# Kernel optimization log

Hardware: AMD Instinct MI355X
Metric: run time of the kernel (lower is better)

## Reference

```python
import jax, jax.numpy as jnp
import numpy as np

B, D, H, W = 512, 32, 128, 128


def setup_inputs() -> dict:
    key = jax.random.key(0)
    k1, k2, k3, k4 = jax.random.split(key, 4)
    inputs = jax.random.uniform(k1, (B, D), dtype=jnp.float32)
    stamp = jax.random.uniform(k2, (H, W, 1), dtype=jnp.float32)
    rows = jax.random.randint(k3, (D,), 0, H)
    cols = jax.random.randint(k4, (D,), 0, W)
    coords = jnp.stack([rows, cols], axis=-1).astype(jnp.int32)  # [D,2]
    return {"inputs": inputs, "stamp": stamp, "coords": coords}


def _static_indices(d, h, w):
    # rows/cols replication counts (static, numpy)
    rows_per = np.full(d, h // d, np.int32); rows_per[: h % d] += 1
    cols_per = np.full(d, w // d, np.int32); cols_per[: w % d] += 1
    # equidistant bar layout
    bar_w = w // (3 * d + 2)
    total_gap = w - d * bar_w
    gap = total_gap // (d + 1)
    extra = total_gap - gap * (d + 1)
    beg = extra // 2
    col_to_bar = np.full(w, -1, np.int32)
    for i in range(d):
        s = beg + i * (bar_w + gap) + gap
        col_to_bar[s : s + bar_w] = i
    return rows_per, cols_per, col_to_bar


def reference(inputs, stamp, coords):
    b, d = inputs.shape
    h, w = stamp.shape[:2]
    rows_per, cols_per, col_to_bar = _static_indices(d, h, w)

    # channel 1: deepinsight scatter (duplicates sum, matching tf.scatter_nd)
    di = jnp.zeros((b, h, w), inputs.dtype).at[:, coords[:, 0], coords[:, 1]].add(inputs)

    # channel 2: row-wise copy
    row_idx = np.repeat(np.arange(d), rows_per)  # [h]
    rowcopy = jnp.broadcast_to(inputs[:, row_idx][:, :, None], (b, h, w))

    # channel 3: normalized pairwise abs distance, expanded to h x w
    dm = jnp.abs(inputs[:, :, None] - inputs[:, None, :])  # [b,d,d]
    mn = jnp.min(dm, axis=(1, 2), keepdims=True)
    mx = jnp.max(dm, axis=(1, 2), keepdims=True)
    nd = (dm - mn) / (mx - mn)
    nd = nd[:, np.repeat(np.arange(d), rows_per), :][:, :, np.repeat(np.arange(d), cols_per)]

    # channel 4: equidistant bar graph (bars fill rows [0, bar_height))
    bar_height = jnp.clip(jnp.round(inputs * h).astype(jnp.int32), 0, h)  # [b,d]
    mask = (jnp.arange(h)[None, :, None] < bar_height[:, None, :]).astype(inputs.dtype)  # [b,h,d]
    safe = np.where(col_to_bar < 0, 0, col_to_bar)
    bars = mask[:, :, safe] * (col_to_bar >= 0).astype(inputs.dtype)[None, None, :]  # [b,h,w]

    stamp_b = jnp.broadcast_to(stamp, (b, h, w, 1))
    return jnp.concatenate(
        [stamp_b, di[..., None], rowcopy[..., None], nd[..., None], bars[..., None]], axis=-1
    )
```

## Files before the change

### kernel.cpp

```cpp
#include <hip/hip_runtime.h>


__global__ __launch_bounds__(256) void di_main(const float* __restrict__ inputs,
                                               const float* __restrict__ stamp,
                                               const int* __restrict__ coords,
                                               float* __restrict__ out) {
    const int blk = blockIdx.x;
    const int b = blk >> 4;
    const int part = blk & 15;
    const int tid = threadIdx.x;

    __shared__ float xs[32];
    __shared__ int bh[32];
    __shared__ float sinv;
    __shared__ float buf[256 * 20];

    if (tid < 64) {
        float v = inputs[b * 32 + (tid & 31)];
        if (tid < 32) {
            xs[tid] = v;
            int t = (int)rintf(v * 128.0f);
            bh[tid] = t < 0 ? 0 : (t > 128 ? 128 : t);
        }
        float mn = v, mx = v;
#pragma unroll
        for (int off = 1; off < 32; off <<= 1) {
            mn = fminf(mn, __shfl_xor(mn, off));
            mx = fmaxf(mx, __shfl_xor(mx, off));
        }
        if (tid == 0) sinv = 1.0f / (mx - mn);
    }
    __syncthreads();

    const float inv = sinv;

    const int lp = part * 1024 + tid * 4;
    const int h = lp >> 7;
    const int w0 = lp & 127;

    const float rowv = xs[h >> 2];
    const float ndv = fabsf(rowv - xs[w0 >> 2]) * inv;

    const float4 sv = *reinterpret_cast<const float4*>(stamp + h * 128 + w0);
    const float svj[4] = {sv.x, sv.y, sv.z, sv.w};

    alignas(16) float vals[20];
#pragma unroll
    for (int j = 0; j < 4; ++j) {
        const int w = w0 + j;
        float barv = 0.0f;
        const int t = w - 17;
        if (t >= 0 && t <= 93 && (t % 3) == 0) {
            const int bar = t / 3;
            barv = (h < bh[bar]) ? 1.0f : 0.0f;
        }
        vals[5 * j + 0] = svj[j];
        vals[5 * j + 1] = 0.0f;
        vals[5 * j + 2] = rowv;
        vals[5 * j + 3] = ndv;
        vals[5 * j + 4] = barv;
    }

    float4* lw = reinterpret_cast<float4*>(&buf[tid * 20]);
    const float4* src = reinterpret_cast<const float4*>(vals);
#pragma unroll
    for (int k = 0; k < 5; ++k) lw[k] = src[k];
    __syncthreads();

    if (tid < 32) {
        const int r = coords[2 * tid], c = coords[2 * tid + 1];
        if ((r >> 3) == part)
            atomicAdd(&buf[((r & 7) * 128 + c) * 5 + 1], xs[tid]);
    }
    __syncthreads();

    float4* dst = reinterpret_cast<float4*>(out + ((size_t)b * 16384 + (size_t)part * 1024) * 5);
    const float4* lr = reinterpret_cast<const float4*>(buf);
#pragma unroll
    for (int it = 0; it < 5; ++it) {
        const int f = it * 256 + tid;
        dst[f] = lr[f];
    }
}

extern "C" void kernel_launch(void* const* d_in, const int* in_sizes, int n_in,
                              void* d_out, int out_size, void* d_ws, size_t ws_size,
                              hipStream_t stream) {
    const float* inputs = (const float*)d_in[0];
    const float* stamp  = (const float*)d_in[1];
    const int*   coords = (const int*)d_in[2];
    float* out = (float*)d_out;

    di_main<<<8192, 256, 0, stream>>>(inputs, stamp, coords, out);
}
```

Baseline: 167.7 us.

## Write interleaved output directly from registers, dropping LDS staging buffer

Removes the 20 KB shared-memory staging buffer. Each thread now computes every output float4 directly by decoding pixel and channel from the flat index, then stores it straight to global memory. Each block covers a quarter-image (20 float4 per thread) instead of 1/16, which cuts the grid from 8192 to 2048 blocks. Duplicate-coordinate scatter adds are done with global atomics after a barrier. The trade is more per-element index arithmetic and branching, plus scalar stamp loads, in exchange for less LDS traffic and higher occupancy. Correctness relies on the global stores being visible to the same block's atomics after __syncthreads.

```diff
diff --git a/kernel.cpp b/kernel.cpp
--- a/kernel.cpp
+++ b/kernel.cpp
@@ -6,14 +6,13 @@
                                                const int* __restrict__ coords,
                                                float* __restrict__ out) {
     const int blk = blockIdx.x;
-    const int b = blk >> 4;
-    const int part = blk & 15;
+    const int b = blk >> 2;
+    const int qt = blk & 3;
     const int tid = threadIdx.x;
 
     __shared__ float xs[32];
     __shared__ int bh[32];
     __shared__ float sinv;
-    __shared__ float buf[256 * 20];
 
     if (tid < 64) {
         float v = inputs[b * 32 + (tid & 31)];
@@ -31,55 +30,52 @@
         if (tid == 0) sinv = 1.0f / (mx - mn);
     }
     __syncthreads();
-
     const float inv = sinv;
 
-    const int lp = part * 1024 + tid * 4;
-    const int h = lp >> 7;
-    const int w0 = lp & 127;
+    float4* outq = reinterpret_cast<float4*>(out) + (size_t)b * 20480 + (size_t)qt * 5120;
 
-    const float rowv = xs[h >> 2];
-    const float ndv = fabsf(rowv - xs[w0 >> 2]) * inv;
+#pragma unroll 2
+    for (int i = 0; i < 20; ++i) {
+        const int q = i * 256 + tid;
+        const unsigned F = (unsigned)(qt * 5120 + q) * 4u;
+        unsigned p = F / 5u;
+        int ch = (int)(F - p * 5u);
 
-    const float4 sv = *reinterpret_cast<const float4*>(stamp + h * 128 + w0);
-    const float svj[4] = {sv.x, sv.y, sv.z, sv.w};
+        float vjs[4];
+#pragma unroll
+        for (int j = 0; j < 4; ++j) {
+            const int h = (int)(p >> 7);
+            const int w = (int)(p & 127u);
+            const float rowv = xs[h >> 2];
+            const float ndv = fabsf(rowv - xs[w >> 2]) * inv;
+            const int t = w - 17;
+            const int bar = t / 3;
+            float barv = 0.0f;
+            if (t >= 0 && t - bar * 3 == 0 && bar < 32)
+                barv = (h < bh[bar]) ? 1.0f : 0.0f;
+            const float sval = stamp[p];
 
-    alignas(16) float vals[20];
-#pragma unroll
-    for (int j = 0; j < 4; ++j) {
-        const int w = w0 + j;
-        float barv = 0.0f;
-        const int t = w - 17;
-        if (t >= 0 && t <= 93 && (t % 3) == 0) {
-            const int bar = t / 3;
-            barv = (h < bh[bar]) ? 1.0f : 0.0f;
+            float val;
+            if (ch == 0)      val = sval;
+            else if (ch == 1) val = 0.0f;
+            else if (ch == 2) val = rowv;
+            else if (ch == 3) val = ndv;
+            else              val = barv;
+            vjs[j] = val;
+
+            ++ch;
+            if (ch == 5) { ch = 0; ++p; }
         }
-        vals[5 * j + 0] = svj[j];
-        vals[5 * j + 1] = 0.0f;
-        vals[5 * j + 2] = rowv;
-        vals[5 * j + 3] = ndv;
-        vals[5 * j + 4] = barv;
+        float4 r;
+        r.x = vjs[0]; r.y = vjs[1]; r.z = vjs[2]; r.w = vjs[3];
+        outq[q] = r;
     }
 
-    float4* lw = reinterpret_cast<float4*>(&buf[tid * 20]);
-    const float4* src = reinterpret_cast<const float4*>(vals);
-#pragma unroll
-    for (int k = 0; k < 5; ++k) lw[k] = src[k];
     __syncthreads();
-
     if (tid < 32) {
         const int r = coords[2 * tid], c = coords[2 * tid + 1];
-        if ((r >> 3) == part)
-            atomicAdd(&buf[((r & 7) * 128 + c) * 5 + 1], xs[tid]);
-    }
-    __syncthreads();
-
-    float4* dst = reinterpret_cast<float4*>(out + ((size_t)b * 16384 + (size_t)part * 1024) * 5);
-    const float4* lr = reinterpret_cast<const float4*>(buf);
-#pragma unroll
-    for (int it = 0; it < 5; ++it) {
-        const int f = it * 256 + tid;
-        dst[f] = lr[f];
+        if ((r >> 5) == qt)
+            atomicAdd(out + ((size_t)b * 16384 + (size_t)(r * 128 + c)) * 5 + 1, xs[tid]);
     }
 }
 
@@ -91,5 +87,5 @@
     const int*   coords = (const int*)d_in[2];
     float* out = (float*)d_out;
 
-    di_main<<<8192, 256, 0, stream>>>(inputs, stamp, coords, out);
+    di_main<<<2048, 256, 0, stream>>>(inputs, stamp, coords, out);
 }
```

New measurement: 199.4 us. +18.9%, slower.

## Process two chunks per block with double-buffered LDS and shuffle-based broadcasts

Applied to the files above, without the earlier changes.

Each block now handles two 1024-pixel chunks, using two LDS buffers so the second chunk is computed while the first is written out. Per-batch values (inputs, bar heights, min/max) are kept in registers and broadcast with wave shuffles rather than through shared memory, which removes the initial barrier. The duplicate-summing scatter now issues global atomics after the stores, with a final block barrier to order them within the block. The grid is halved, which lowers occupancy, and the global atomics rely on that block-level ordering against its own earlier stores.

```diff
diff --git a/kernel.cpp b/kernel.cpp
--- a/kernel.cpp
+++ b/kernel.cpp
@@ -6,80 +6,80 @@
                                                const int* __restrict__ coords,
                                                float* __restrict__ out) {
     const int blk = blockIdx.x;
-    const int b = blk >> 4;
-    const int part = blk & 15;
+    const int b = blk >> 3;
+    const int part = blk & 7;
     const int tid = threadIdx.x;
+    const int lane = tid & 63;
 
-    __shared__ float xs[32];
-    __shared__ int bh[32];
-    __shared__ float sinv;
-    __shared__ float buf[256 * 20];
+    __shared__ float buf[2][256 * 20];
 
-    if (tid < 64) {
-        float v = inputs[b * 32 + (tid & 31)];
-        if (tid < 32) {
-            xs[tid] = v;
-            int t = (int)rintf(v * 128.0f);
-            bh[tid] = t < 0 ? 0 : (t > 128 ? 128 : t);
+    const float v = inputs[b * 32 + (lane & 31)];
+    int bt = (int)rintf(v * 128.0f);
+    bt = bt < 0 ? 0 : (bt > 128 ? 128 : bt);
+    float mn = v, mx = v;
+#pragma unroll
+    for (int off = 1; off < 32; off <<= 1) {
+        mn = fminf(mn, __shfl_xor(mn, off));
+        mx = fmaxf(mx, __shfl_xor(mx, off));
+    }
+    const float inv = 1.0f / (mx - mn);
+
+    auto compute = [&](int c, float* vals) {
+        const int lp = part * 2048 + c * 1024 + tid * 4;
+        const int h = lp >> 7;
+        const int w0 = lp & 127;
+        const float rowv = __shfl(v, h >> 2);
+        const float ndv = fabsf(rowv - __shfl(v, w0 >> 2)) * inv;
+        const float4 sv = *reinterpret_cast<const float4*>(stamp + h * 128 + w0);
+        const float svj[4] = {sv.x, sv.y, sv.z, sv.w};
+#pragma unroll
+        for (int j = 0; j < 4; ++j) {
+            const int w = w0 + j;
+            const int t = w - 17;
+            const int bar = t / 3;
+            const bool valid = (t >= 0) && (t <= 93) && (t - bar * 3 == 0);
+            const int bhv = __shfl(bt, valid ? bar : 0);
+            const float barv = (valid && h < bhv) ? 1.0f : 0.0f;
+            vals[5 * j + 0] = svj[j];
+            vals[5 * j + 1] = 0.0f;
+            vals[5 * j + 2] = rowv;
+            vals[5 * j + 3] = ndv;
+            vals[5 * j + 4] = barv;
         }
-        float mn = v, mx = v;
+    };
+    auto stage = [&](int c, const float* vals) {
+        float4* lw = reinterpret_cast<float4*>(&buf[c][tid * 20]);
+        const float4* src = reinterpret_cast<const float4*>(vals);
 #pragma unroll
-        for (int off = 1; off < 32; off <<= 1) {
-            mn = fminf(mn, __shfl_xor(mn, off));
-            mx = fmaxf(mx, __shfl_xor(mx, off));
+        for (int k = 0; k < 5; ++k) lw[k] = src[k];
+    };
+    auto flush = [&](int c) {
+        float4* dst = reinterpret_cast<float4*>(out) +
+                      (size_t)b * 20480 + (size_t)part * 2560 + (size_t)c * 1280;
+        const float4* lr = reinterpret_cast<const float4*>(buf[c]);
+#pragma unroll
+        for (int it = 0; it < 5; ++it) {
+            const int f = it * 256 + tid;
+            dst[f] = lr[f];
         }
-        if (tid == 0) sinv = 1.0f / (mx - mn);
-    }
+    };
+
+    alignas(16) float valsA[20], valsB[20];
+    compute(0, valsA);
+    stage(0, valsA);
     __syncthreads();
+    compute(1, valsB);
+    stage(1, valsB);
+    flush(0);
+    __syncthreads();
+    flush(1);
 
-    const float inv = sinv;
-
-    const int lp = part * 1024 + tid * 4;
-    const int h = lp >> 7;
-    const int w0 = lp & 127;
-
-    const float rowv = xs[h >> 2];
-    const float ndv = fabsf(rowv - xs[w0 >> 2]) * inv;
-
-    const float4 sv = *reinterpret_cast<const float4*>(stamp + h * 128 + w0);
-    const float svj[4] = {sv.x, sv.y, sv.z, sv.w};
-
-    alignas(16) float vals[20];
-#pragma unroll
-    for (int j = 0; j < 4; ++j) {
-        const int w = w0 + j;
-        float barv = 0.0f;
-        const int t = w - 17;
-        if (t >= 0 && t <= 93 && (t % 3) == 0) {
-            const int bar = t / 3;
-            barv = (h < bh[bar]) ? 1.0f : 0.0f;
-        }
-        vals[5 * j + 0] = svj[j];
-        vals[5 * j + 1] = 0.0f;
-        vals[5 * j + 2] = rowv;
-        vals[5 * j + 3] = ndv;
-        vals[5 * j + 4] = barv;
-    }
-
-    float4* lw = reinterpret_cast<float4*>(&buf[tid * 20]);
-    const float4* src = reinterpret_cast<const float4*>(vals);
-#pragma unroll
-    for (int k = 0; k < 5; ++k) lw[k] = src[k];
     __syncthreads();
-
     if (tid < 32) {
         const int r = coords[2 * tid], c = coords[2 * tid + 1];
-        if ((r >> 3) == part)
-            atomicAdd(&buf[((r & 7) * 128 + c) * 5 + 1], xs[tid]);
-    }
-    __syncthreads();
-
-    float4* dst = reinterpret_cast<float4*>(out + ((size_t)b * 16384 + (size_t)part * 1024) * 5);
-    const float4* lr = reinterpret_cast<const float4*>(buf);
-#pragma unroll
-    for (int it = 0; it < 5; ++it) {
-        const int f = it * 256 + tid;
-        dst[f] = lr[f];
+        if ((r >> 4) == part)
+            atomicAdd(out + ((size_t)b * 16384 + (size_t)(r * 128 + c)) * 5 + 1,
+                      __shfl(v, tid));
     }
 }
 
@@ -91,5 +91,5 @@
     const int*   coords = (const int*)d_in[2];
     float* out = (float*)d_out;
 
-    di_main<<<8192, 256, 0, stream>>>(inputs, stamp, coords, out);
+    di_main<<<4096, 256, 0, stream>>>(inputs, stamp, coords, out);
 }
```

Measured after the change: 166.2 us. Within noise of the previous version (-0.9%).
